# Performance work log

Measured on AMD Instinct MI355X. Metric: run time of the kernel, lower is better.

Reference implementation:

```python
import jax, jax.numpy as jnp
import numpy as np

N_NODES = 10000
N_EDGES = 640000
IN_CH = 128
OUT_CH = 128


def setup_inputs() -> dict:
    key = jax.random.key(0)
    k1, k2, k3, k4 = jax.random.split(key, 4)
    x = jax.random.normal(k1, (N_NODES, IN_CH), dtype=jnp.float32)
    edge_index = jax.random.randint(k2, (2, N_EDGES), 0, N_NODES, dtype=jnp.int64)
    # nn.Linear(2*in_channels, out_channels): weight [out, 2*in], bias [out]
    bound = 1.0 / np.sqrt(2 * IN_CH)
    W = jax.random.uniform(k3, (OUT_CH, 2 * IN_CH), dtype=jnp.float32, minval=-bound, maxval=bound)
    b = jax.random.uniform(k4, (OUT_CH,), dtype=jnp.float32, minval=-bound, maxval=bound)
    return {"x": x, "W": W, "b": b, "edge_index": edge_index}


def reference(x, W, b, edge_index):
    # PyG convention: edge_index[0] = source j, edge_index[1] = target i
    src, dst = edge_index[0], edge_index[1]
    x_i = x[dst]                      # [E, C] target features
    x_j = x[src]                      # [E, C] source features
    feat = jnp.concatenate([x_i, x_j - x_i], axis=-1)  # [E, 2C]
    msg = feat @ W.T + b              # [E, out]
    out = jax.ops.segment_max(msg, dst, num_segments=x.shape[0])  # [N, out]
    # isolated nodes: PyG scatter-max yields 0, segment_max yields -inf
    return jnp.where(jnp.isfinite(out), out, 0.0)
```

## Files before the change

kernel.cpp:

```cpp
#include <hip/hip_runtime.h>
#include <math.h>

#define N_CH 128
#define NB_MAX 512
#define ECHUNK 2048
#define GCHUNK 2048

__global__ __launch_bounds__(256) void prep_kernel(const float* __restrict__ W,
                                                   float* __restrict__ V1,
                                                   float* __restrict__ V2,
                                                   int* __restrict__ binCount,
                                                   int* __restrict__ binCursor,
                                                   int nb) {
    int i = blockIdx.x * 256 + threadIdx.x;
    if (i < N_CH * N_CH) {
        int k = i >> 7, o = i & 127;
        float w1 = W[o * 256 + k];
        float w2 = W[o * 256 + 128 + k];
        V1[i] = w1 - w2;
        V2[i] = w2;
    }
    if (i < nb) { binCount[i] = 0; binCursor[i] = 0; }
}

__global__ __launch_bounds__(256) void gemm_kernel(const float* __restrict__ x,
                                                   const float* __restrict__ V1,
                                                   const float* __restrict__ V2,
                                                   const float* __restrict__ bias,
                                                   const int* __restrict__ dst,
                                                   float* __restrict__ A,
                                                   unsigned short* __restrict__ Bh,
                                                   int* __restrict__ binCount,
                                                   int n_nodes, int n_edges, int nb) {
    __shared__ float xs[32][N_CH];
    __shared__ int h[NB_MAX];
    const int tid = threadIdx.x;
    const int bid = blockIdx.x;

    const int ebase = bid * ECHUNK;
    const int ecnt = min(ECHUNK, n_edges - ebase);
    for (int i = tid; i < nb; i += 256) h[i] = 0;
    __syncthreads();
    if (ecnt > 0) {
        const int j = tid * 8;
        if (j + 8 <= ecnt) {
            int4 d0 = *(const int4*)(dst + ebase + j);
            int4 d1 = *(const int4*)(dst + ebase + j + 4);
            atomicAdd(&h[d0.x >> 5], 1); atomicAdd(&h[d0.y >> 5], 1);
            atomicAdd(&h[d0.z >> 5], 1); atomicAdd(&h[d0.w >> 5], 1);
            atomicAdd(&h[d1.x >> 5], 1); atomicAdd(&h[d1.y >> 5], 1);
            atomicAdd(&h[d1.z >> 5], 1); atomicAdd(&h[d1.w >> 5], 1);
        } else {
            for (int q = j; q < min(j + 8, ecnt); ++q)
                atomicAdd(&h[dst[ebase + q] >> 5], 1);
        }
    }
    __syncthreads();
    for (int i = tid; i < nb; i += 256)
        if (h[i]) atomicAdd(&binCount[i], h[i]);

    const int n0 = bid * 32;
    if (n0 >= n_nodes) return;

    if (n0 + 32 <= n_nodes) {
        const float4* xg = (const float4*)(x + (size_t)n0 * N_CH);
        float4* xsv = (float4*)&xs[0][0];
        #pragma unroll
        for (int i = 0; i < 4; ++i) xsv[tid + i * 256] = xg[tid + i * 256];
    } else {
        for (int i = tid; i < 32 * N_CH; i += 256) {
            int n = n0 + (i >> 7);
            (&xs[0][0])[i] = (n < n_nodes) ? x[(size_t)n * N_CH + (i & 127)] : 0.f;
        }
    }
    __syncthreads();

    const int o  = tid & 127;
    const int nh = tid >> 7;
    const float bo = bias[o];
    float acc1[16], acc2[16];
    #pragma unroll
    for (int i = 0; i < 16; ++i) { acc1[i] = 0.f; acc2[i] = 0.f; }

    const float* xrow = &xs[nh * 16][0];
    for (int k4 = 0; k4 < N_CH; k4 += 4) {
        float w1[4], w2[4];
        #pragma unroll
        for (int j = 0; j < 4; ++j) {
            w1[j] = V1[(k4 + j) * N_CH + o];
            w2[j] = V2[(k4 + j) * N_CH + o];
        }
        #pragma unroll
        for (int i = 0; i < 16; ++i) {
            float4 xv = *(const float4*)&xrow[i * N_CH + k4];
            acc1[i] = fmaf(xv.x, w1[0], acc1[i]); acc2[i] = fmaf(xv.x, w2[0], acc2[i]);
            acc1[i] = fmaf(xv.y, w1[1], acc1[i]); acc2[i] = fmaf(xv.y, w2[1], acc2[i]);
            acc1[i] = fmaf(xv.z, w1[2], acc1[i]); acc2[i] = fmaf(xv.z, w2[2], acc2[i]);
            acc1[i] = fmaf(xv.w, w1[3], acc1[i]); acc2[i] = fmaf(xv.w, w2[3], acc2[i]);
        }
    }

    #pragma unroll
    for (int i = 0; i < 16; ++i) {
        int n = n0 + nh * 16 + i;
        if (n < n_nodes) {
            A[(size_t)n * N_CH + o] = acc1[i] + bo;
            unsigned int bits = __float_as_uint(acc2[i]);
            unsigned int r = (bits + 0x7FFFu + ((bits >> 16) & 1u)) >> 16;
            Bh[(size_t)n * N_CH + o] = (unsigned short)r;
        }
    }
}

__global__ __launch_bounds__(256) void bin_kernel(const int* __restrict__ src,
                                                  const int* __restrict__ dst,
                                                  const int* __restrict__ binCount,
                                                  int* __restrict__ binCursor,
                                                  int* __restrict__ binOffG,
                                                  unsigned int* __restrict__ binned,
                                                  int n_edges, int nb) {
    __shared__ int sc[512];
    __shared__ int bOff[512];
    const int tid = threadIdx.x;
    const int base = blockIdx.x * ECHUNK;
    const int cnt = min(ECHUNK, n_edges - base);

    int c0 = (tid < nb) ? binCount[tid] : 0;
    int c1 = (tid + 256 < nb) ? binCount[tid + 256] : 0;
    int p0 = (c0 + 3) & ~3, p1 = (c1 + 3) & ~3;
    sc[tid] = p0; sc[tid + 256] = p1;
    __syncthreads();
    #pragma unroll
    for (int off = 1; off < 512; off <<= 1) {
        int u0 = (tid >= off) ? sc[tid - off] : 0;
        int u1 = sc[tid + 256 - off];
        __syncthreads();
        sc[tid] += u0; sc[tid + 256] += u1;
        __syncthreads();
    }
    bOff[tid] = sc[tid] - p0;
    bOff[tid + 256] = sc[tid + 256] - p1;
    if (blockIdx.x == 0) {
        if (tid < nb) binOffG[tid] = bOff[tid];
        if (tid + 256 < nb) binOffG[tid + 256] = bOff[tid + 256];
    }
    sc[tid] = 0; sc[tid + 256] = 0;
    __syncthreads();

    const int myb = tid * 8;
    const int mycnt = max(0, min(8, cnt - myb));
    unsigned int pk[8]; int bb[8], rr[8];
    if (mycnt == 8) {
        int4 s0 = *(const int4*)(src + base + myb);
        int4 s1 = *(const int4*)(src + base + myb + 4);
        int4 d0 = *(const int4*)(dst + base + myb);
        int4 d1 = *(const int4*)(dst + base + myb + 4);
        int sv[8] = {s0.x, s0.y, s0.z, s0.w, s1.x, s1.y, s1.z, s1.w};
        int dv[8] = {d0.x, d0.y, d0.z, d0.w, d1.x, d1.y, d1.z, d1.w};
        #pragma unroll
        for (int k = 0; k < 8; ++k) {
            int b = dv[k] >> 5;
            pk[k] = ((unsigned int)(dv[k] & 31) << 14) | (unsigned int)sv[k];
            bb[k] = b;
            rr[k] = atomicAdd(&sc[b], 1);
        }
    } else {
        for (int k = 0; k < mycnt; ++k) {
            int s = src[base + myb + k];
            int d = dst[base + myb + k];
            int b = d >> 5;
            pk[k] = ((unsigned int)(d & 31) << 14) | (unsigned int)s;
            bb[k] = b;
            rr[k] = atomicAdd(&sc[b], 1);
        }
    }
    __syncthreads();

    for (int i = tid; i < nb; i += 256) {
        int c = sc[i];
        if (c) bOff[i] += atomicAdd(&binCursor[i], c);
    }
    __syncthreads();

    for (int k = 0; k < mycnt; ++k)
        binned[bOff[bb[k]] + rr[k]] = pk[k];
}

#define FOLD4(acc_lo, acc_hi, a, b, c, d)                                        \
    acc_lo = fmaxf(acc_lo, fmaxf(fmaxf(__uint_as_float((a) << 16),               \
                                       __uint_as_float((b) << 16)),              \
                                 fmaxf(__uint_as_float((c) << 16),               \
                                       __uint_as_float((d) << 16))));            \
    acc_hi = fmaxf(acc_hi, fmaxf(fmaxf(__uint_as_float((a) & 0xFFFF0000u),       \
                                       __uint_as_float((b) & 0xFFFF0000u)),      \
                                 fmaxf(__uint_as_float((c) & 0xFFFF0000u),       \
                                       __uint_as_float((d) & 0xFFFF0000u))));

__global__ __launch_bounds__(512) void gather_kernel(
        const float* __restrict__ A,
        const uint4* __restrict__ Bh4,
        const int* __restrict__ binOffG,
        const int* __restrict__ binCount,
        const unsigned int* __restrict__ binned,
        float* __restrict__ out,
        int n_nodes) {
    __shared__ int lidx[GCHUNK];
    __shared__ int h32[32], e33[33];
    const int b = blockIdx.x;
    const int tid = threadIdx.x;
    const int wv  = tid >> 6;
    const int l   = tid & 63;
    const int sub = l >> 4;
    const int col = l & 15;
    const int rbeg = binOffG[b];
    const int cnt  = binCount[b];

    float mlo[4][4], mhi[4][4]; int tcnt[4];
    #pragma unroll
    for (int i = 0; i < 4; ++i) {
        tcnt[i] = 0;
        #pragma unroll
        for (int u = 0; u < 4; ++u) { mlo[i][u] = -INFINITY; mhi[i][u] = -INFINITY; }
    }

    for (int cb = 0; cb < cnt; cb += GCHUNK) {
        const int ccnt = min(GCHUNK, cnt - cb);
        if (tid < 32) h32[tid] = 0;
        __syncthreads();

        const int mb = tid * 4;
        const int mc = max(0, min(4, ccnt - mb));
        int myd[4], mys[4], myr[4];
        if (mc == 4) {
            int4 r4 = *(const int4*)((const int*)binned + rbeg + cb + mb);
            unsigned int wv4[4] = {(unsigned int)r4.x, (unsigned int)r4.y,
                                   (unsigned int)r4.z, (unsigned int)r4.w};
            #pragma unroll
            for (int k = 0; k < 4; ++k) {
                myd[k] = (int)(wv4[k] >> 14);
                mys[k] = (int)(wv4[k] & 16383u);
                myr[k] = atomicAdd(&h32[myd[k]], 1);
            }
        } else {
            for (int k = 0; k < mc; ++k) {
                unsigned int w = binned[rbeg + cb + mb + k];
                myd[k] = (int)(w >> 14);
                mys[k] = (int)(w & 16383u);
                myr[k] = atomicAdd(&h32[myd[k]], 1);
            }
        }
        __syncthreads();
        if (tid == 0) {
            int s = 0;
            #pragma unroll
            for (int k = 0; k < 32; ++k) { e33[k] = s; s += h32[k]; }
            e33[32] = s;
        }
        __syncthreads();
        for (int k = 0; k < mc; ++k)
            lidx[e33[myd[k]] + myr[k]] = mys[k];
        __syncthreads();

        #pragma unroll
        for (int i = 0; i < 4; ++i) {
            const int nl = wv * 4 + i;
            const int c  = h32[nl];
            const int bg = e33[nl];
            tcnt[i] += c;
            int q = 0;
            for (; q + 16 <= c; q += 16) {
                int e0 = lidx[bg + q + sub];
                int e1 = lidx[bg + q + 4 + sub];
                int e2 = lidx[bg + q + 8 + sub];
                int e3 = lidx[bg + q + 12 + sub];
                uint4 w0 = Bh4[(size_t)e0 * 16 + col];
                uint4 w1 = Bh4[(size_t)e1 * 16 + col];
                uint4 w2 = Bh4[(size_t)e2 * 16 + col];
                uint4 w3 = Bh4[(size_t)e3 * 16 + col];
                FOLD4(mlo[i][0], mhi[i][0], w0.x, w1.x, w2.x, w3.x);
                FOLD4(mlo[i][1], mhi[i][1], w0.y, w1.y, w2.y, w3.y);
                FOLD4(mlo[i][2], mhi[i][2], w0.z, w1.z, w2.z, w3.z);
                FOLD4(mlo[i][3], mhi[i][3], w0.w, w1.w, w2.w, w3.w);
            }
            for (; q < c; q += 4) {
                int r = q + sub;
                if (r < c) {
                    uint4 w = Bh4[(size_t)lidx[bg + r] * 16 + col];
                    mlo[i][0] = fmaxf(mlo[i][0], __uint_as_float(w.x << 16));
                    mhi[i][0] = fmaxf(mhi[i][0], __uint_as_float(w.x & 0xFFFF0000u));
                    mlo[i][1] = fmaxf(mlo[i][1], __uint_as_float(w.y << 16));
                    mhi[i][1] = fmaxf(mhi[i][1], __uint_as_float(w.y & 0xFFFF0000u));
                    mlo[i][2] = fmaxf(mlo[i][2], __uint_as_float(w.z << 16));
                    mhi[i][2] = fmaxf(mhi[i][2], __uint_as_float(w.z & 0xFFFF0000u));
                    mlo[i][3] = fmaxf(mlo[i][3], __uint_as_float(w.w << 16));
                    mhi[i][3] = fmaxf(mhi[i][3], __uint_as_float(w.w & 0xFFFF0000u));
                }
            }
        }
        __syncthreads();
    }

    #pragma unroll
    for (int i = 0; i < 4; ++i) {
        const int n = b * 32 + wv * 4 + i;
        if (n >= n_nodes) continue;
        float lo[4], hi[4];
        #pragma unroll
        for (int u = 0; u < 4; ++u) {
            lo[u] = mlo[i][u]; hi[u] = mhi[i][u];
            lo[u] = fmaxf(lo[u], __shfl_xor(lo[u], 16, 64));
            hi[u] = fmaxf(hi[u], __shfl_xor(hi[u], 16, 64));
            lo[u] = fmaxf(lo[u], __shfl_xor(lo[u], 32, 64));
            hi[u] = fmaxf(hi[u], __shfl_xor(hi[u], 32, 64));
        }
        if (sub == 0) {
            float r8[8];
            if (tcnt[i] > 0) {
                const float4* Arow = (const float4*)(A + (size_t)n * N_CH + col * 8);
                float4 a0 = Arow[0], a1 = Arow[1];
                r8[0] = a0.x + lo[0]; r8[1] = a0.y + hi[0];
                r8[2] = a0.z + lo[1]; r8[3] = a0.w + hi[1];
                r8[4] = a1.x + lo[2]; r8[5] = a1.y + hi[2];
                r8[6] = a1.z + lo[3]; r8[7] = a1.w + hi[3];
            } else {
                #pragma unroll
                for (int j = 0; j < 8; ++j) r8[j] = 0.f;
            }
            float4* orow = (float4*)(out + (size_t)n * N_CH + col * 8);
            orow[0] = make_float4(r8[0], r8[1], r8[2], r8[3]);
            orow[1] = make_float4(r8[4], r8[5], r8[6], r8[7]);
        }
    }
}

extern "C" void kernel_launch(void* const* d_in, const int* in_sizes, int n_in,
                              void* d_out, int out_size, void* d_ws, size_t ws_size,
                              hipStream_t stream) {
    const float* x = (const float*)d_in[0];
    const float* W = (const float*)d_in[1];
    const float* b = (const float*)d_in[2];
    const int*   ei = (const int*)d_in[3];

    const int n_nodes = in_sizes[0] / N_CH;
    const int n_edges = in_sizes[3] / 2;
    const int nb = (n_nodes + 31) >> 5;
    const int* src = ei;
    const int* dst = ei + n_edges;
    float* out = (float*)d_out;

    char* ws = (char*)d_ws;
    size_t off = 0;
    auto alloc = [&](size_t bytes) -> void* {
        void* p = ws + off;
        off += (bytes + 255) & ~(size_t)255;
        return p;
    };
    float* V1        = (float*)alloc((size_t)N_CH * N_CH * 4);
    float* V2        = (float*)alloc((size_t)N_CH * N_CH * 4);
    float* A         = (float*)alloc((size_t)n_nodes * N_CH * 4);
    unsigned short* Bh = (unsigned short*)alloc((size_t)n_nodes * N_CH * 2);
    int*   binCount  = (int*)alloc((size_t)nb * 4);
    int*   binCursor = (int*)alloc((size_t)nb * 4);
    int*   binOffG   = (int*)alloc((size_t)nb * 4);
    unsigned int* binned = (unsigned int*)alloc(((size_t)n_edges + 4 * NB_MAX) * 4);
    (void)ws_size; (void)n_in; (void)out_size;

    const int nodeBlocks = (n_nodes + 31) / 32;
    const int edgeBlocks = (n_edges + ECHUNK - 1) / ECHUNK;
    const int ng = max(nodeBlocks, edgeBlocks);

    prep_kernel  <<<64, 256, 0, stream>>>(W, V1, V2, binCount, binCursor, nb);
    gemm_kernel  <<<ng, 256, 0, stream>>>(x, V1, V2, b, dst, A, Bh, binCount,
                                          n_nodes, n_edges, nb);
    bin_kernel   <<<edgeBlocks, 256, 0, stream>>>(src, dst, binCount, binCursor,
                                                  binOffG, binned, n_edges, nb);
    gather_kernel<<<nb, 512, 0, stream>>>(A, (const uint4*)Bh, binOffG, binCount,
                                          binned, out, n_nodes);
}
```

Measured before the change: 136.6 us.

## Halve gather bin size to 16 nodes and vectorize weight loads in GEMM

Destination bins shrink from 32 to 16 nodes, which doubles the bin count to about 625 and doubles the number of gather blocks. Each gather block is now 256 threads and each thread handles 8 edge records. The bin prefix scan is reworked so each thread scans 4 slots, supporting up to 1024 bins. Separately, V1/V2 are stored in a k-interleaved layout so the GEMM loads each group of four weights with a single float4. The aim is better gather occupancy and load balance plus fewer GEMM load instructions, at the cost of more bins and more padding in the binned array.

```diff
diff --git a/kernel.cpp b/kernel.cpp
--- a/kernel.cpp
+++ b/kernel.cpp
@@ -2,7 +2,7 @@
 #include <math.h>
 
 #define N_CH 128
-#define NB_MAX 512
+#define NB_MAX 1024
 #define ECHUNK 2048
 #define GCHUNK 2048
 
@@ -17,8 +17,9 @@
         int k = i >> 7, o = i & 127;
         float w1 = W[o * 256 + k];
         float w2 = W[o * 256 + 128 + k];
-        V1[i] = w1 - w2;
-        V2[i] = w2;
+        int ip = (k >> 2) * 512 + o * 4 + (k & 3);
+        V1[ip] = w1 - w2;
+        V2[ip] = w2;
     }
     if (i < nb) { binCount[i] = 0; binCursor[i] = 0; }
 }
@@ -46,13 +47,13 @@
         if (j + 8 <= ecnt) {
             int4 d0 = *(const int4*)(dst + ebase + j);
             int4 d1 = *(const int4*)(dst + ebase + j + 4);
-            atomicAdd(&h[d0.x >> 5], 1); atomicAdd(&h[d0.y >> 5], 1);
-            atomicAdd(&h[d0.z >> 5], 1); atomicAdd(&h[d0.w >> 5], 1);
-            atomicAdd(&h[d1.x >> 5], 1); atomicAdd(&h[d1.y >> 5], 1);
-            atomicAdd(&h[d1.z >> 5], 1); atomicAdd(&h[d1.w >> 5], 1);
+            atomicAdd(&h[d0.x >> 4], 1); atomicAdd(&h[d0.y >> 4], 1);
+            atomicAdd(&h[d0.z >> 4], 1); atomicAdd(&h[d0.w >> 4], 1);
+            atomicAdd(&h[d1.x >> 4], 1); atomicAdd(&h[d1.y >> 4], 1);
+            atomicAdd(&h[d1.z >> 4], 1); atomicAdd(&h[d1.w >> 4], 1);
         } else {
             for (int q = j; q < min(j + 8, ecnt); ++q)
-                atomicAdd(&h[dst[ebase + q] >> 5], 1);
+                atomicAdd(&h[dst[ebase + q] >> 4], 1);
         }
     }
     __syncthreads();
@@ -84,19 +85,15 @@
 
     const float* xrow = &xs[nh * 16][0];
     for (int k4 = 0; k4 < N_CH; k4 += 4) {
-        float w1[4], w2[4];
-        #pragma unroll
-        for (int j = 0; j < 4; ++j) {
-            w1[j] = V1[(k4 + j) * N_CH + o];
-            w2[j] = V2[(k4 + j) * N_CH + o];
-        }
+        float4 w1 = *(const float4*)(V1 + k4 * 128 + o * 4);
+        float4 w2 = *(const float4*)(V2 + k4 * 128 + o * 4);
         #pragma unroll
         for (int i = 0; i < 16; ++i) {
             float4 xv = *(const float4*)&xrow[i * N_CH + k4];
-            acc1[i] = fmaf(xv.x, w1[0], acc1[i]); acc2[i] = fmaf(xv.x, w2[0], acc2[i]);
-            acc1[i] = fmaf(xv.y, w1[1], acc1[i]); acc2[i] = fmaf(xv.y, w2[1], acc2[i]);
-            acc1[i] = fmaf(xv.z, w1[2], acc1[i]); acc2[i] = fmaf(xv.z, w2[2], acc2[i]);
-            acc1[i] = fmaf(xv.w, w1[3], acc1[i]); acc2[i] = fmaf(xv.w, w2[3], acc2[i]);
+            acc1[i] = fmaf(xv.x, w1.x, acc1[i]); acc2[i] = fmaf(xv.x, w2.x, acc2[i]);
+            acc1[i] = fmaf(xv.y, w1.y, acc1[i]); acc2[i] = fmaf(xv.y, w2.y, acc2[i]);
+            acc1[i] = fmaf(xv.z, w1.z, acc1[i]); acc2[i] = fmaf(xv.z, w2.z, acc2[i]);
+            acc1[i] = fmaf(xv.w, w1.w, acc1[i]); acc2[i] = fmaf(xv.w, w2.w, acc2[i]);
         }
     }
 
@@ -119,32 +116,45 @@
                                                   int* __restrict__ binOffG,
                                                   unsigned int* __restrict__ binned,
                                                   int n_edges, int nb) {
-    __shared__ int sc[512];
-    __shared__ int bOff[512];
+    __shared__ int sc[256];
+    __shared__ int hist[NB_MAX];
+    __shared__ int bOff[NB_MAX];
     const int tid = threadIdx.x;
     const int base = blockIdx.x * ECHUNK;
     const int cnt = min(ECHUNK, n_edges - base);
 
-    int c0 = (tid < nb) ? binCount[tid] : 0;
-    int c1 = (tid + 256 < nb) ? binCount[tid + 256] : 0;
-    int p0 = (c0 + 3) & ~3, p1 = (c1 + 3) & ~3;
-    sc[tid] = p0; sc[tid + 256] = p1;
-    __syncthreads();
-    #pragma unroll
-    for (int off = 1; off < 512; off <<= 1) {
-        int u0 = (tid >= off) ? sc[tid - off] : 0;
-        int u1 = sc[tid + 256 - off];
-        __syncthreads();
-        sc[tid] += u0; sc[tid + 256] += u1;
-        __syncthreads();
-    }
-    bOff[tid] = sc[tid] - p0;
-    bOff[tid + 256] = sc[tid + 256] - p1;
+    int p[4]; int s = 0;
+    #pragma unroll
+    for (int k = 0; k < 4; ++k) {
+        int slot = tid * 4 + k;
+        int c = (slot < nb) ? binCount[slot] : 0;
+        p[k] = (c + 3) & ~3;
+        s += p[k];
+    }
+    sc[tid] = s;
+    __syncthreads();
+    #pragma unroll
+    for (int off = 1; off < 256; off <<= 1) {
+        int u = (tid >= off) ? sc[tid - off] : 0;
+        __syncthreads();
+        sc[tid] += u;
+        __syncthreads();
+    }
+    int run = sc[tid] - s;
+    #pragma unroll
+    for (int k = 0; k < 4; ++k) {
+        int slot = tid * 4 + k;
+        bOff[slot] = run;
+        run += p[k];
+    }
     if (blockIdx.x == 0) {
-        if (tid < nb) binOffG[tid] = bOff[tid];
-        if (tid + 256 < nb) binOffG[tid + 256] = bOff[tid + 256];
-    }
-    sc[tid] = 0; sc[tid + 256] = 0;
+        #pragma unroll
+        for (int k = 0; k < 4; ++k) {
+            int slot = tid * 4 + k;
+            if (slot < nb) binOffG[slot] = bOff[slot];
+        }
+    }
+    for (int i = tid; i < NB_MAX; i += 256) hist[i] = 0;
     __syncthreads();
 
     const int myb = tid * 8;
@@ -159,25 +169,25 @@
         int dv[8] = {d0.x, d0.y, d0.z, d0.w, d1.x, d1.y, d1.z, d1.w};
         #pragma unroll
         for (int k = 0; k < 8; ++k) {
-            int b = dv[k] >> 5;
-            pk[k] = ((unsigned int)(dv[k] & 31) << 14) | (unsigned int)sv[k];
+            int b = dv[k] >> 4;
+            pk[k] = ((unsigned int)(dv[k] & 15) << 14) | (unsigned int)sv[k];
             bb[k] = b;
-            rr[k] = atomicAdd(&sc[b], 1);
+            rr[k] = atomicAdd(&hist[b], 1);
         }
     } else {
         for (int k = 0; k < mycnt; ++k) {
-            int s = src[base + myb + k];
-            int d = dst[base + myb + k];
-            int b = d >> 5;
-            pk[k] = ((unsigned int)(d & 31) << 14) | (unsigned int)s;
+            int sv = src[base + myb + k];
+            int dv = dst[base + myb + k];
+            int b = dv >> 4;
+            pk[k] = ((unsigned int)(dv & 15) << 14) | (unsigned int)sv;
             bb[k] = b;
-            rr[k] = atomicAdd(&sc[b], 1);
+            rr[k] = atomicAdd(&hist[b], 1);
         }
     }
     __syncthreads();
 
     for (int i = tid; i < nb; i += 256) {
-        int c = sc[i];
+        int c = hist[i];
         if (c) bOff[i] += atomicAdd(&binCursor[i], c);
     }
     __syncthreads();
@@ -196,7 +206,7 @@
                                  fmaxf(__uint_as_float((c) & 0xFFFF0000u),       \
                                        __uint_as_float((d) & 0xFFFF0000u))));
 
-__global__ __launch_bounds__(512) void gather_kernel(
+__global__ __launch_bounds__(256) void gather_kernel(
         const float* __restrict__ A,
         const uint4* __restrict__ Bh4,
         const int* __restrict__ binOffG,
@@ -205,7 +215,7 @@
         float* __restrict__ out,
         int n_nodes) {
     __shared__ int lidx[GCHUNK];
-    __shared__ int h32[32], e33[33];
+    __shared__ int h16[16], e17[17];
     const int b = blockIdx.x;
     const int tid = threadIdx.x;
     const int wv  = tid >> 6;
@@ -225,47 +235,50 @@
 
     for (int cb = 0; cb < cnt; cb += GCHUNK) {
         const int ccnt = min(GCHUNK, cnt - cb);
-        if (tid < 32) h32[tid] = 0;
-        __syncthreads();
-
-        const int mb = tid * 4;
-        const int mc = max(0, min(4, ccnt - mb));
-        int myd[4], mys[4], myr[4];
-        if (mc == 4) {
-            int4 r4 = *(const int4*)((const int*)binned + rbeg + cb + mb);
-            unsigned int wv4[4] = {(unsigned int)r4.x, (unsigned int)r4.y,
-                                   (unsigned int)r4.z, (unsigned int)r4.w};
+        if (tid < 16) h16[tid] = 0;
+        __syncthreads();
+
+        const int mb = tid * 8;
+        const int mc = max(0, min(8, ccnt - mb));
+        int myd[8], mys[8], myr[8];
+        if (mc == 8) {
+            int4 r0 = *(const int4*)((const int*)binned + rbeg + cb + mb);
+            int4 r1 = *(const int4*)((const int*)binned + rbeg + cb + mb + 4);
+            unsigned int wv8[8] = {(unsigned int)r0.x, (unsigned int)r0.y,
+                                   (unsigned int)r0.z, (unsigned int)r0.w,
+                                   (unsigned int)r1.x, (unsigned int)r1.y,
+                                   (unsigned int)r1.z, (unsigned int)r1.w};
             #pragma unroll
-            for (int k = 0; k < 4; ++k) {
-                myd[k] = (int)(wv4[k] >> 14);
-                mys[k] = (int)(wv4[k] & 16383u);
-                myr[k] = atomicAdd(&h32[myd[k]], 1);
+            for (int k = 0; k < 8; ++k) {
+                myd[k] = (int)(wv8[k] >> 14);
+                mys[k] = (int)(wv8[k] & 16383u);
+                myr[k] = atomicAdd(&h16[myd[k]], 1);
             }
         } else {
             for (int k = 0; k < mc; ++k) {
                 unsigned int w = binned[rbeg + cb + mb + k];
                 myd[k] = (int)(w >> 14);
                 mys[k] = (int)(w & 16383u);
-                myr[k] = atomicAdd(&h32[myd[k]], 1);
+                myr[k] = atomicAdd(&h16[myd[k]], 1);
             }
         }
         __syncthreads();
         if (tid == 0) {
             int s = 0;
             #pragma unroll
-            for (int k = 0; k < 32; ++k) { e33[k] = s; s += h32[k]; }
-            e33[32] = s;
+            for (int k = 0; k < 16; ++k) { e17[k] = s; s += h16[k]; }
+            e17[16] = s;
         }
         __syncthreads();
         for (int k = 0; k < mc; ++k)
-            lidx[e33[myd[k]] + myr[k]] = mys[k];
+            lidx[e17[myd[k]] + myr[k]] = mys[k];
         __syncthreads();
 
         #pragma unroll
         for (int i = 0; i < 4; ++i) {
             const int nl = wv * 4 + i;
-            const int c  = h32[nl];
-            const int bg = e33[nl];
+            const int c  = h16[nl];
+            const int bg = e17[nl];
             tcnt[i] += c;
             int q = 0;
             for (; q + 16 <= c; q += 16) {
@@ -302,7 +315,7 @@
 
     #pragma unroll
     for (int i = 0; i < 4; ++i) {
-        const int n = b * 32 + wv * 4 + i;
+        const int n = b * 16 + wv * 4 + i;
         if (n >= n_nodes) continue;
         float lo[4], hi[4];
         #pragma unroll
@@ -343,7 +356,7 @@
 
     const int n_nodes = in_sizes[0] / N_CH;
     const int n_edges = in_sizes[3] / 2;
-    const int nb = (n_nodes + 31) >> 5;
+    const int nb = (n_nodes + 15) >> 4;
     const int* src = ei;
     const int* dst = ei + n_edges;
     float* out = (float*)d_out;
@@ -374,6 +387,6 @@
                                           n_nodes, n_edges, nb);
     bin_kernel   <<<edgeBlocks, 256, 0, stream>>>(src, dst, binCount, binCursor,
                                                   binOffG, binned, n_edges, nb);
-    gather_kernel<<<nb, 512, 0, stream>>>(A, (const uint4*)Bh, binOffG, binCount,
+    gather_kernel<<<nb, 256, 0, stream>>>(A, (const uint4*)Bh, binOffG, binCount,
                                           binned, out, n_nodes);
 }
```

Measured after the change: 133.8 us. 2.0% less time.
